# Kernel optimization log

Hardware: AMD Instinct MI355X
Metric: run time of the kernel (lower is better)

The kernel has to match this reference:

```python
import jax, jax.numpy as jnp
import numpy as np

N_NODES = 50000
N_EDGES = 800000
NFEAT = 512
NHID = 64
NHEADS = 8
NCLASS = 40
ALPHA = 0.2  # LeakyReLU slope
EPS = 1e-16  # guards isolated-node division


def setup_inputs() -> dict:
    key = jax.random.key(0)
    k = jax.random.split(key, 6)
    x = jax.random.normal(k[0], (N_NODES, NFEAT), dtype=jnp.float32)
    W_heads = jax.random.normal(k[1], (NHEADS, NFEAT, NHID), dtype=jnp.float32) * 0.05
    a_heads = jax.random.normal(k[2], (NHEADS, 2 * NHID), dtype=jnp.float32) * 0.05
    W_out = jax.random.normal(k[3], (NHEADS * NHID, NCLASS), dtype=jnp.float32) * 0.05
    a_out = jax.random.normal(k[4], (2 * NCLASS,), dtype=jnp.float32) * 0.05
    edge_index = jax.random.randint(k[5], (2, N_EDGES), 0, N_NODES, dtype=jnp.int32)
    return {"x": x, "W_heads": W_heads, "a_heads": a_heads,
            "W_out": W_out, "a_out": a_out, "edge_index": edge_index}


def _gat_layer(x, W, a, row, col, concat):
    # pyGAT sparse layer: h = xW; e_ij = exp(-LeakyReLU(a^T [h_i || h_j]));
    # out_i = sum_j e_ij h_j / sum_j e_ij   (aggregate into row, gather from col)
    D = W.shape[1]
    h = x @ W                                            # [N, D]
    score = h[row] @ a[:D] + h[col] @ a[D:]              # [E]
    e = jnp.exp(-jax.nn.leaky_relu(score, ALPHA))        # [E]
    num = jax.ops.segment_sum(e[:, None] * h[col], row, num_segments=x.shape[0])  # [N, D]
    den = jax.ops.segment_sum(e, row, num_segments=x.shape[0])                    # [N]
    out = num / (den[:, None] + EPS)
    return jax.nn.elu(out) if concat else out


def reference(x, W_heads, a_heads, W_out, a_out, edge_index):
    # dropout layers are identity in eval mode (training=False)
    row, col = edge_index[0], edge_index[1]
    heads = jax.vmap(lambda W, a: _gat_layer(x, W, a, row, col, True))(W_heads, a_heads)
    # [H, N, D] -> [N, H*D] (concat along feature dim, head-major like torch.cat)
    hcat = jnp.transpose(heads, (1, 0, 2)).reshape(x.shape[0], -1)
    return _gat_layer(hcat, W_out, a_out, row, col, False)  # [N, NCLASS]
```

## Files before the change

### kernel.cpp

```cpp
#include <hip/hip_runtime.h>
#include <hip/hip_bf16.h>

#define N_NODES 50000
#define N_EDGES 800000
#define NFEAT   512
#define NHID    64
#define NHEADS  8
#define NCLASS  40
#define HD      (NHEADS*NHID)
#define ALPHA   0.2f
#define EPS_F   1e-16f
#define NCHUNK  ((N_NODES + 255)/256)

typedef __attribute__((ext_vector_type(8))) short short8;
typedef __attribute__((ext_vector_type(4))) float floatx4;

__device__ __forceinline__ float bf2f(unsigned short u) {
    union { unsigned int i; float f; } v; v.i = ((unsigned int)u) << 16; return v.f;
}
__device__ __forceinline__ unsigned short f2bf(float f) {
    union { __hip_bfloat16 h; unsigned short u; } cv;
    cv.h = __float2bfloat16(f);
    return cv.u;
}

__device__ __forceinline__ void gload16(const unsigned short* g, short* l) {
    __builtin_amdgcn_global_load_lds(
        (const __attribute__((address_space(1))) void*)g,
        (__attribute__((address_space(3))) void*)l,
        16, 0, 0);
}

__global__ __launch_bounds__(256) void convx(const float* __restrict__ x,
                                             unsigned short* __restrict__ xb) {
    int i = blockIdx.x*256 + threadIdx.x;
    if (i >= N_NODES*64) return;
    const float* s = x + (size_t)i*8;
    float4 a = *(const float4*)s, b = *(const float4*)(s+4);
    short8 h;
    h[0] = (short)f2bf(a.x); h[1] = (short)f2bf(a.y);
    h[2] = (short)f2bf(a.z); h[3] = (short)f2bf(a.w);
    h[4] = (short)f2bf(b.x); h[5] = (short)f2bf(b.y);
    h[6] = (short)f2bf(b.z); h[7] = (short)f2bf(b.w);
    *(short8*)(xb + (size_t)i*8) = h;
}

__global__ void prep(const float* __restrict__ Wh, unsigned short* __restrict__ Wrb,
                     const float* __restrict__ Wo, unsigned short* __restrict__ Wob,
                     int* __restrict__ deg) {
    int idx = blockIdx.x*256 + threadIdx.x;
    if (idx >= 512*512) return;
    if (idx < N_NODES) deg[idx] = 0;
    {
        int n = idx >> 9, k = idx & 511;
        int hd = n >> 6, d = n & 63;
        Wrb[idx] = f2bf(Wh[(size_t)hd*NFEAT*NHID + (size_t)k*NHID + d]);
    }
    if (idx < 64*512) {
        int n = idx >> 9, k = idx & 511;
        float v = (n < NCLASS) ? Wo[(size_t)k*NCLASS + n] : 0.f;
        Wob[idx] = f2bf(v);
    }
}

__global__ __launch_bounds__(256) void mfma_gemm1(const unsigned short* __restrict__ Abf,
                                                  const unsigned short* __restrict__ Bbf,
                                                  const float* __restrict__ a_heads,
                                                  unsigned short* __restrict__ H1p,
                                                  float* __restrict__ srcdot,
                                                  float* __restrict__ dstdot, int M) {
    int id = blockIdx.x;
    int rb = (id >> 5)*8 + (id & 7);
    int cb = (id >> 3) & 3;
    int row0 = rb * 128, col0 = cb * 128;
    if (row0 >= M) return;

    __shared__ short Asl[128*32];
    __shared__ short Bsl[128*32];
    int tid  = threadIdx.x;
    int wid  = tid >> 6, lane = tid & 63;
    int lrow = lane & 15, quad = lane >> 4;
    int wm = wid & 1, wn = wid >> 1;

    int srow = wid*16 + (lane >> 2);
    int skk  = (lane & 3) * 8;
    int ar0 = row0 + srow;      ar0 = ar0 < M ? ar0 : M - 1;
    int ar1 = row0 + 64 + srow; ar1 = ar1 < M ? ar1 : M - 1;
    const unsigned short* ag0 = Abf + (size_t)ar0*512 + skk;
    const unsigned short* ag1 = Abf + (size_t)ar1*512 + skk;
    const unsigned short* bg0 = Bbf + (size_t)(col0 + srow)*512 + skk;
    const unsigned short* bg1 = Bbf + (size_t)(col0 + 64 + srow)*512 + skk;
    short* al0 = &Asl[(wid*16)*32];
    short* al1 = &Asl[(64 + wid*16)*32];
    short* bl0 = &Bsl[(wid*16)*32];
    short* bl1 = &Bsl[(64 + wid*16)*32];

    floatx4 acc[4][4];
#pragma unroll
    for (int mm = 0; mm < 4; mm++)
#pragma unroll
        for (int nn = 0; nn < 4; nn++) acc[mm][nn] = (floatx4){0.f,0.f,0.f,0.f};

    for (int k0 = 0; k0 < 512; k0 += 32) {
        gload16(ag0 + k0, al0);
        gload16(ag1 + k0, al1);
        gload16(bg0 + k0, bl0);
        gload16(bg1 + k0, bl1);
        __syncthreads();
        short8 af[4], bfr[4];
#pragma unroll
        for (int mm = 0; mm < 4; ++mm)
            af[mm] = *(const short8*)(&Asl[(wm*64 + mm*16 + lrow)*32 + quad*8]);
#pragma unroll
        for (int nn = 0; nn < 4; ++nn)
            bfr[nn] = *(const short8*)(&Bsl[(wn*64 + nn*16 + lrow)*32 + quad*8]);
#pragma unroll
        for (int mm = 0; mm < 4; ++mm)
#pragma unroll
            for (int nn = 0; nn < 4; ++nn)
                acc[mm][nn] = __builtin_amdgcn_mfma_f32_16x16x32_bf16(
                    af[mm], bfr[nn], acc[mm][nn], 0, 0, 0);
        __syncthreads();
    }

    {
        int head = (col0 >> 6) + wn;
        float a0v[4], a1v[4];
#pragma unroll
        for (int nn = 0; nn < 4; ++nn) {
            a0v[nn] = a_heads[head*128 + nn*16 + lrow];
            a1v[nn] = a_heads[head*128 + 64 + nn*16 + lrow];
        }
#pragma unroll
        for (int mm = 0; mm < 4; ++mm) {
#pragma unroll
            for (int r = 0; r < 4; ++r) {
                float s0 = 0.f, s1 = 0.f;
#pragma unroll
                for (int nn = 0; nn < 4; ++nn) {
                    float v = acc[mm][nn][r];
                    s0 = fmaf(v, a0v[nn], s0);
                    s1 = fmaf(v, a1v[nn], s1);
                }
#pragma unroll
                for (int off = 1; off < 16; off <<= 1) {
                    s0 += __shfl_xor(s0, off, 64);
                    s1 += __shfl_xor(s1, off, 64);
                }
                int grow = row0 + wm*64 + mm*16 + quad*4 + r;
                if (lrow == 0 && grow < M) {
                    srcdot[(size_t)grow*8 + head] = s0;
                    dstdot[(size_t)grow*8 + head] = s1;
                }
            }
        }
    }

#pragma unroll
    for (int mm = 0; mm < 4; ++mm) {
        int rbase = row0 + wm*64 + mm*16 + quad*4;
#pragma unroll
        for (int nn = 0; nn < 4; ++nn) {
            int c = col0 + wn*64 + nn*16 + lrow;
            int off = (c & 63)*8 + (c >> 6);
#pragma unroll
            for (int r = 0; r < 4; ++r) {
                int grow = rbase + r;
                if (grow < M)
                    H1p[(size_t)grow*512 + off] = f2bf(acc[mm][nn][r]);
            }
        }
    }
}

__global__ __launch_bounds__(512) void mfma_gemm2(const unsigned short* __restrict__ Abf,
                                                  const unsigned short* __restrict__ Bbf,
                                                  const float* __restrict__ a_out,
                                                  float* __restrict__ H2p,
                                                  float* __restrict__ src2,
                                                  float* __restrict__ dst2, int M) {
    __shared__ short Asl[128*32];
    __shared__ short Bsl[64*32];
    int tid  = threadIdx.x;
    int wid  = tid >> 6, lane = tid & 63;
    int lrow = lane & 15, quad = lane >> 4;
    int row0 = blockIdx.x * 128;
    if (row0 >= M) return;

    int srow = wid*16 + (lane >> 2);
    int skk  = (lane & 3) * 8;
    int ar = row0 + srow; ar = ar < M ? ar : M - 1;
    const unsigned short* ag = Abf + (size_t)ar*512 + skk;
    const unsigned short* bg = Bbf + (size_t)srow*512 + skk;
    short* al = &Asl[(wid*16)*32];
    short* bl = &Bsl[(wid*16)*32];

    floatx4 acc[4];
#pragma unroll
    for (int nn = 0; nn < 4; nn++) acc[nn] = (floatx4){0.f,0.f,0.f,0.f};

    for (int k0 = 0; k0 < 512; k0 += 32) {
        gload16(ag + k0, al);
        if (wid < 4) gload16(bg + k0, bl);
        __syncthreads();
        short8 af, bfr[4];
        af = *(const short8*)(&Asl[(wid*16 + lrow)*32 + quad*8]);
#pragma unroll
        for (int nn = 0; nn < 4; ++nn)
            bfr[nn] = *(const short8*)(&Bsl[(nn*16 + lrow)*32 + quad*8]);
#pragma unroll
        for (int nn = 0; nn < 4; ++nn)
            acc[nn] = __builtin_amdgcn_mfma_f32_16x16x32_bf16(
                af, bfr[nn], acc[nn], 0, 0, 0);
        __syncthreads();
    }

    {
        float a0v[4], a1v[4];
#pragma unroll
        for (int nn = 0; nn < 4; ++nn) {
            int c = nn*16 + lrow;
            a0v[nn] = c < NCLASS ? a_out[c] : 0.f;
            a1v[nn] = c < NCLASS ? a_out[NCLASS + c] : 0.f;
        }
#pragma unroll
        for (int r = 0; r < 4; ++r) {
            float s0 = 0.f, s1 = 0.f;
#pragma unroll
            for (int nn = 0; nn < 4; ++nn) {
                float v = acc[nn][r];
                s0 = fmaf(v, a0v[nn], s0);
                s1 = fmaf(v, a1v[nn], s1);
            }
#pragma unroll
            for (int off = 1; off < 16; off <<= 1) {
                s0 += __shfl_xor(s0, off, 64);
                s1 += __shfl_xor(s1, off, 64);
            }
            int grow = row0 + wid*16 + quad*4 + r;
            if (lrow == 0 && grow < M) {
                src2[grow] = s0;
                dst2[grow] = s1;
            }
        }
    }

#pragma unroll
    for (int nn = 0; nn < 4; ++nn) {
        int c = nn*16 + lrow;
#pragma unroll
        for (int r = 0; r < 4; ++r) {
            int grow = row0 + wid*16 + quad*4 + r;
            if (grow < M)
                H2p[(size_t)grow*64 + c] = acc[nn][r];
        }
    }
}

__global__ void histk(const int* __restrict__ row, int* __restrict__ deg) {
    int e = blockIdx.x*256 + threadIdx.x;
    if (e < N_EDGES) atomicAdd(&deg[row[e]], 1);
}
__global__ void scanA(const int* __restrict__ deg, int* __restrict__ row_ptr,
                      int* __restrict__ chunk_tot) {
    __shared__ int s[256];
    int t = threadIdx.x;
    int idx = blockIdx.x*256 + t;
    int v = (idx < N_NODES) ? deg[idx] : 0;
    s[t] = v;
    __syncthreads();
#pragma unroll
    for (int off = 1; off < 256; off <<= 1) {
        int x = (t >= off) ? s[t-off] : 0;
        __syncthreads();
        s[t] += x;
        __syncthreads();
    }
    if (idx < N_NODES) row_ptr[idx] = s[t] - v;
    if (t == 255) chunk_tot[blockIdx.x] = s[t];
}
__global__ void scanB(const int* __restrict__ chunk_tot, int* __restrict__ chunk_off,
                      int* __restrict__ row_ptr) {
    __shared__ int s[256];
    int t = threadIdx.x;
    int v = (t < NCHUNK) ? chunk_tot[t] : 0;
    s[t] = v;
    __syncthreads();
#pragma unroll
    for (int off = 1; off < 256; off <<= 1) {
        int x = (t >= off) ? s[t-off] : 0;
        __syncthreads();
        s[t] += x;
        __syncthreads();
    }
    if (t < NCHUNK) chunk_off[t] = s[t] - v;
    if (t == 255) row_ptr[N_NODES] = s[t];
}
__global__ void scanC(const int* __restrict__ chunk_off, int* __restrict__ row_ptr,
                      int* __restrict__ cursor) {
    int idx = blockIdx.x*256 + threadIdx.x;
    if (idx < N_NODES) {
        int rp = row_ptr[idx] + chunk_off[idx >> 8];
        row_ptr[idx] = rp;
        cursor[idx] = rp;
    }
}

__global__ void fillk_w1(const int* __restrict__ row, const int* __restrict__ col,
                         const float* __restrict__ srcdot, const float* __restrict__ dstdot,
                         int* __restrict__ cursor, int* __restrict__ csr_col,
                         float* __restrict__ Wcsr) {
    int e = blockIdx.x*256 + threadIdx.x;
    if (e >= N_EDGES) return;
    int r = row[e], c = col[e];
    int pos = atomicAdd(&cursor[r], 1);
    csr_col[pos] = c;
    float4 sa = *(const float4*)(srcdot + (size_t)r*8);
    float4 sb = *(const float4*)(srcdot + (size_t)r*8 + 4);
    float4 da = *(const float4*)(dstdot + (size_t)c*8);
    float4 db = *(const float4*)(dstdot + (size_t)c*8 + 4);
    float s[8] = {sa.x+da.x, sa.y+da.y, sa.z+da.z, sa.w+da.w,
                  sb.x+db.x, sb.y+db.y, sb.z+db.z, sb.w+db.w};
    float o[8];
#pragma unroll
    for (int j = 0; j < 8; j++) {
        float lr = s[j] > 0.f ? s[j] : ALPHA*s[j];
        o[j] = __expf(-lr);
    }
    *(float4*)(Wcsr + (size_t)pos*8)     = make_float4(o[0], o[1], o[2], o[3]);
    *(float4*)(Wcsr + (size_t)pos*8 + 4) = make_float4(o[4], o[5], o[6], o[7]);
}

__global__ __launch_bounds__(256) void agg1(const unsigned short* __restrict__ H1p,
                                            const float* __restrict__ Wcsr,
                                            const int* __restrict__ row_ptr,
                                            const int* __restrict__ csr_col,
                                            unsigned short* __restrict__ hcatb) {
    int wave = (blockIdx.x*256 + threadIdx.x) >> 6;
    int lane = threadIdx.x & 63;
    if (wave >= N_NODES) return;
    int start = row_ptr[wave], end = row_ptr[wave+1];
    float acc[8], den[8];
#pragma unroll
    for (int j = 0; j < 8; j++) { acc[j] = 0.f; den[j] = 0.f; }

    int k = start;
    for (; k + 4 <= end; k += 4) {
        int c0 = csr_col[k],   c1 = csr_col[k+1];
        int c2 = csr_col[k+2], c3 = csr_col[k+3];
        short8 hv0 = *(const short8*)(H1p + (size_t)c0*512 + lane*8);
        short8 hv1 = *(const short8*)(H1p + (size_t)c1*512 + lane*8);
        short8 hv2 = *(const short8*)(H1p + (size_t)c2*512 + lane*8);
        short8 hv3 = *(const short8*)(H1p + (size_t)c3*512 + lane*8);
        float4 wv[8];
#pragma unroll
        for (int q = 0; q < 8; q++)
            wv[q] = *(const float4*)(Wcsr + (size_t)k*8 + q*4);
        const float* w0 = (const float*)&wv[0];
        const float* w1 = (const float*)&wv[2];
        const float* w2 = (const float*)&wv[4];
        const float* w3 = (const float*)&wv[6];
#pragma unroll
        for (int j = 0; j < 8; j++) {
            den[j] += (w0[j] + w1[j]) + (w2[j] + w3[j]);
            acc[j] = fmaf(w0[j], bf2f((unsigned short)hv0[j]), acc[j]);
            acc[j] = fmaf(w1[j], bf2f((unsigned short)hv1[j]), acc[j]);
            acc[j] = fmaf(w2[j], bf2f((unsigned short)hv2[j]), acc[j]);
            acc[j] = fmaf(w3[j], bf2f((unsigned short)hv3[j]), acc[j]);
        }
    }
    for (; k < end; ++k) {
        int c = csr_col[k];
        float4 wa = *(const float4*)(Wcsr + (size_t)k*8);
        float4 wb = *(const float4*)(Wcsr + (size_t)k*8 + 4);
        short8 hv = *(const short8*)(H1p + (size_t)c*512 + lane*8);
        float w[8] = {wa.x, wa.y, wa.z, wa.w, wb.x, wb.y, wb.z, wb.w};
#pragma unroll
        for (int j = 0; j < 8; j++) {
            den[j] += w[j];
            acc[j] = fmaf(w[j], bf2f((unsigned short)hv[j]), acc[j]);
        }
    }
#pragma unroll
    for (int j = 0; j < 8; j++) {
        float o = acc[j] / (den[j] + EPS_F);
        o = o > 0.f ? o : (__expf(o) - 1.f);
        hcatb[(size_t)wave*HD + j*64 + lane] = f2bf(o);
    }
}

__global__ __launch_bounds__(256) void agg2(const float* __restrict__ H2p,
                                            const float* __restrict__ src2,
                                            const float* __restrict__ dst2,
                                            const int* __restrict__ row_ptr,
                                            const int* __restrict__ csr_col,
                                            float* __restrict__ out) {
    int wave = (blockIdx.x*256 + threadIdx.x) >> 6;
    int lane = threadIdx.x & 63;
    if (wave >= N_NODES) return;
    int start = row_ptr[wave], end = row_ptr[wave+1];
    int deg = end - start;
    float s2i = src2[wave];
    int l = lane < NCLASS ? lane : 0;
    float acc = 0.f, den = 0.f;

    int colreg = 0;
    if (deg > 0) colreg = csr_col[start + (lane < deg ? lane : deg - 1)];

#define AG2_G1(T, H, IDX) do { \
    int cg_ = __builtin_amdgcn_readlane(colreg, (IDX)); \
    T = dst2[cg_]; \
    H = H2p[(size_t)cg_*64 + l]; \
} while(0)
#define AG2_C1(T, H) do { \
    float t_ = s2i + (T); \
    t_ = t_ > 0.f ? t_ : ALPHA*t_; \
    float w_ = __expf(-t_); \
    den += w_; acc = fmaf(w_, (H), acc); \
} while(0)
#define AG2_G8(T0,T1,T2,T3,T4,T5,T6,T7,H0,H1,H2,H3,H4,H5,H6,H7,BASE) do { \
    AG2_G1(T0,H0,(BASE));   AG2_G1(T1,H1,(BASE)+1); \
    AG2_G1(T2,H2,(BASE)+2); AG2_G1(T3,H3,(BASE)+3); \
    AG2_G1(T4,H4,(BASE)+4); AG2_G1(T5,H5,(BASE)+5); \
    AG2_G1(T6,H6,(BASE)+6); AG2_G1(T7,H7,(BASE)+7); \
} while(0)
#define AG2_C8(T0,T1,T2,T3,T4,T5,T6,T7,H0,H1,H2,H3,H4,H5,H6,H7) do { \
    AG2_C1(T0,H0); AG2_C1(T1,H1); AG2_C1(T2,H2); AG2_C1(T3,H3); \
    AG2_C1(T4,H4); AG2_C1(T5,H5); AG2_C1(T6,H6); AG2_C1(T7,H7); \
} while(0)

    int lim = deg < 64 ? deg : 64;
    int nb = lim >> 3;
    int k = start;
    float ta0,ta1,ta2,ta3,ta4,ta5,ta6,ta7, ga0,ga1,ga2,ga3,ga4,ga5,ga6,ga7;
    float tb0,tb1,tb2,tb3,tb4,tb5,tb6,tb7, gb0,gb1,gb2,gb3,gb4,gb5,gb6,gb7;
    if (nb > 0) {
        AG2_G8(ta0,ta1,ta2,ta3,ta4,ta5,ta6,ta7, ga0,ga1,ga2,ga3,ga4,ga5,ga6,ga7, 0);
        int b = 1;
        for (; b + 1 < nb; b += 2) {
            AG2_G8(tb0,tb1,tb2,tb3,tb4,tb5,tb6,tb7, gb0,gb1,gb2,gb3,gb4,gb5,gb6,gb7, b*8);
            AG2_C8(ta0,ta1,ta2,ta3,ta4,ta5,ta6,ta7, ga0,ga1,ga2,ga3,ga4,ga5,ga6,ga7);
            AG2_G8(ta0,ta1,ta2,ta3,ta4,ta5,ta6,ta7, ga0,ga1,ga2,ga3,ga4,ga5,ga6,ga7, (b+1)*8);
            AG2_C8(tb0,tb1,tb2,tb3,tb4,tb5,tb6,tb7, gb0,gb1,gb2,gb3,gb4,gb5,gb6,gb7);
        }
        if (b < nb) {
            AG2_G8(tb0,tb1,tb2,tb3,tb4,tb5,tb6,tb7, gb0,gb1,gb2,gb3,gb4,gb5,gb6,gb7, b*8);
            AG2_C8(ta0,ta1,ta2,ta3,ta4,ta5,ta6,ta7, ga0,ga1,ga2,ga3,ga4,ga5,ga6,ga7);
            AG2_C8(tb0,tb1,tb2,tb3,tb4,tb5,tb6,tb7, gb0,gb1,gb2,gb3,gb4,gb5,gb6,gb7);
        } else {
            AG2_C8(ta0,ta1,ta2,ta3,ta4,ta5,ta6,ta7, ga0,ga1,ga2,ga3,ga4,ga5,ga6,ga7);
        }
        k = start + nb*8;
    }
    for (; k < end; ++k) {
        int c_ = (k - start < 64) ? __builtin_amdgcn_readlane(colreg, k - start)
                                  : csr_col[k];
        float t = dst2[c_];
        float h = H2p[(size_t)c_*64 + l];
        AG2_C1(t, h);
    }
#undef AG2_G1
#undef AG2_C1
#undef AG2_G8
#undef AG2_C8

    if (lane < NCLASS)
        out[(size_t)wave*NCLASS + lane] = acc / (den + EPS_F);
}

extern "C" void kernel_launch(void* const* d_in, const int* in_sizes, int n_in,
                              void* d_out, int out_size, void* d_ws, size_t ws_size,
                              hipStream_t stream) {
    const float* x       = (const float*)d_in[0];
    const float* W_heads = (const float*)d_in[1];
    const float* a_heads = (const float*)d_in[2];
    const float* W_out   = (const float*)d_in[3];
    const float* a_out   = (const float*)d_in[4];
    const int*   ei      = (const int*)d_in[5];
    const int*   row     = ei;
    const int*   col     = ei + N_EDGES;
    float* out = (float*)d_out;

    char* ws = (char*)d_ws;
    size_t off = 0;
    auto alloc = [&](size_t bytes) {
        char* p = ws + off;
        off = (off + bytes + 255) & ~(size_t)255;
        return p;
    };
    unsigned short* Wrb   = (unsigned short*)alloc((size_t)512*512*2);
    unsigned short* Wob   = (unsigned short*)alloc((size_t)64*512*2);
    unsigned short* H1p   = (unsigned short*)alloc((size_t)N_NODES*HD*2);
    unsigned short* xb    = (unsigned short*)alloc((size_t)N_NODES*NFEAT*2);
    unsigned short* hcatb = xb;
    float* srcdot  = (float*)alloc((size_t)N_NODES*NHEADS*4);
    float* dstdot  = (float*)alloc((size_t)N_NODES*NHEADS*4);
    float* Wcsr    = (float*)alloc((size_t)N_EDGES*NHEADS*4);
    int*   deg     = (int*)alloc((size_t)N_NODES*4);
    int*   row_ptr = (int*)alloc((size_t)(N_NODES+1)*4);
    int*   cursor  = (int*)alloc((size_t)N_NODES*4);
    int*   ctot    = (int*)alloc(256*4);
    int*   coff    = (int*)alloc(256*4);
    int*   csr_col = (int*)alloc((size_t)N_EDGES*4);
    float* H2p     = (float*)alloc((size_t)N_NODES*64*4);
    float* src2    = (float*)alloc((size_t)N_NODES*4);
    float* dst2    = (float*)alloc((size_t)N_NODES*4);
    (void)ws_size;

    const int EB = (N_EDGES + 255)/256;
    const int WB = (N_NODES*64 + 255)/256;

    prep<<<(512*512 + 255)/256, 256, 0, stream>>>(W_heads, Wrb, W_out, Wob, deg);
    convx<<<(N_NODES*64 + 255)/256, 256, 0, stream>>>(x, xb);
    {
        int rtiles = (N_NODES + 127)/128;
        int nblk = ((rtiles + 7)/8) * 32;
        mfma_gemm1<<<nblk, 256, 0, stream>>>(xb, Wrb, a_heads, H1p,
                                             srcdot, dstdot, N_NODES);
    }

    histk<<<EB, 256, 0, stream>>>(row, deg);
    scanA<<<NCHUNK, 256, 0, stream>>>(deg, row_ptr, ctot);
    scanB<<<1, 256, 0, stream>>>(ctot, coff, row_ptr);
    scanC<<<NCHUNK, 256, 0, stream>>>(coff, row_ptr, cursor);
    fillk_w1<<<EB, 256, 0, stream>>>(row, col, srcdot, dstdot, cursor,
                                     csr_col, Wcsr);

    agg1<<<WB, 256, 0, stream>>>(H1p, Wcsr, row_ptr, csr_col, hcatb);

    mfma_gemm2<<<(N_NODES + 127)/128, 512, 0, stream>>>(hcatb, Wob, a_out,
                                                        H2p, src2, dst2, N_NODES);
    agg2<<<WB, 256, 0, stream>>>(H2p, src2, dst2, row_ptr, csr_col, out);
}
```

Measured before the change: 509.0 us.

## Store H1 head-major, give each agg1 lane one head, fuse convx into prep

The GEMM1 epilogue now writes H1 in natural head-major column order instead of an interleaved per-lane layout. In agg1 each lane handles 8 contiguous features of a single head, so it loads only one attention weight per edge instead of eight. It also keeps one denominator and one reciprocal instead of eight divisions, and writes its output as a single 16-byte vector store. The x-to-bf16 conversion is merged into the prep kernel to save a launch, and the gemm2 B-tile LDS pointer is clamped with wid&3 for the waves that skip the B load.

```diff
diff --git a/kernel.cpp b/kernel.cpp
--- a/kernel.cpp
+++ b/kernel.cpp
@@ -31,27 +31,26 @@
         16, 0, 0);
 }
 
-__global__ __launch_bounds__(256) void convx(const float* __restrict__ x,
-                                             unsigned short* __restrict__ xb) {
-    int i = blockIdx.x*256 + threadIdx.x;
-    if (i >= N_NODES*64) return;
-    const float* s = x + (size_t)i*8;
-    float4 a = *(const float4*)s, b = *(const float4*)(s+4);
-    short8 h;
-    h[0] = (short)f2bf(a.x); h[1] = (short)f2bf(a.y);
-    h[2] = (short)f2bf(a.z); h[3] = (short)f2bf(a.w);
-    h[4] = (short)f2bf(b.x); h[5] = (short)f2bf(b.y);
-    h[6] = (short)f2bf(b.z); h[7] = (short)f2bf(b.w);
-    *(short8*)(xb + (size_t)i*8) = h;
-}
-
-__global__ void prep(const float* __restrict__ Wh, unsigned short* __restrict__ Wrb,
-                     const float* __restrict__ Wo, unsigned short* __restrict__ Wob,
-                     int* __restrict__ deg) {
+__global__ __launch_bounds__(256) void prep(const float* __restrict__ x,
+                                            unsigned short* __restrict__ xb,
+                                            const float* __restrict__ Wh,
+                                            unsigned short* __restrict__ Wrb,
+                                            const float* __restrict__ Wo,
+                                            unsigned short* __restrict__ Wob,
+                                            int* __restrict__ deg) {
     int idx = blockIdx.x*256 + threadIdx.x;
-    if (idx >= 512*512) return;
+    if (idx < N_NODES*64) {
+        const float* s = x + (size_t)idx*8;
+        float4 a = *(const float4*)s, b = *(const float4*)(s+4);
+        short8 h;
+        h[0] = (short)f2bf(a.x); h[1] = (short)f2bf(a.y);
+        h[2] = (short)f2bf(a.z); h[3] = (short)f2bf(a.w);
+        h[4] = (short)f2bf(b.x); h[5] = (short)f2bf(b.y);
+        h[6] = (short)f2bf(b.z); h[7] = (short)f2bf(b.w);
+        *(short8*)(xb + (size_t)idx*8) = h;
+    }
     if (idx < N_NODES) deg[idx] = 0;
-    {
+    if (idx < 512*512) {
         int n = idx >> 9, k = idx & 511;
         int hd = n >> 6, d = n & 63;
         Wrb[idx] = f2bf(Wh[(size_t)hd*NFEAT*NHID + (size_t)k*NHID + d]);
@@ -66,7 +65,7 @@
 __global__ __launch_bounds__(256) void mfma_gemm1(const unsigned short* __restrict__ Abf,
                                                   const unsigned short* __restrict__ Bbf,
                                                   const float* __restrict__ a_heads,
-                                                  unsigned short* __restrict__ H1p,
+                                                  unsigned short* __restrict__ H1,
                                                   float* __restrict__ srcdot,
                                                   float* __restrict__ dstdot, int M) {
     int id = blockIdx.x;
@@ -160,14 +159,14 @@
     for (int mm = 0; mm < 4; ++mm) {
         int rbase = row0 + wm*64 + mm*16 + quad*4;
 #pragma unroll
-        for (int nn = 0; nn < 4; ++nn) {
-            int c = col0 + wn*64 + nn*16 + lrow;
-            int off = (c & 63)*8 + (c >> 6);
-#pragma unroll
-            for (int r = 0; r < 4; ++r) {
-                int grow = rbase + r;
-                if (grow < M)
-                    H1p[(size_t)grow*512 + off] = f2bf(acc[mm][nn][r]);
+        for (int r = 0; r < 4; ++r) {
+            int grow = rbase + r;
+            if (grow < M) {
+#pragma unroll
+                for (int nn = 0; nn < 4; ++nn) {
+                    int c = col0 + wn*64 + nn*16 + lrow;
+                    H1[(size_t)grow*512 + c] = f2bf(acc[mm][nn][r]);
+                }
             }
         }
     }
@@ -193,7 +192,7 @@
     const unsigned short* ag = Abf + (size_t)ar*512 + skk;
     const unsigned short* bg = Bbf + (size_t)srow*512 + skk;
     short* al = &Asl[(wid*16)*32];
-    short* bl = &Bsl[(wid*16)*32];
+    short* bl = &Bsl[((wid & 3)*16)*32];
 
     floatx4 acc[4];
 #pragma unroll
@@ -331,7 +330,7 @@
     *(float4*)(Wcsr + (size_t)pos*8 + 4) = make_float4(o[4], o[5], o[6], o[7]);
 }
 
-__global__ __launch_bounds__(256) void agg1(const unsigned short* __restrict__ H1p,
+__global__ __launch_bounds__(256) void agg1(const unsigned short* __restrict__ H1,
                                             const float* __restrict__ Wcsr,
                                             const int* __restrict__ row_ptr,
                                             const int* __restrict__ csr_col,
@@ -340,53 +339,51 @@
     int lane = threadIdx.x & 63;
     if (wave >= N_NODES) return;
     int start = row_ptr[wave], end = row_ptr[wave+1];
-    float acc[8], den[8];
-#pragma unroll
-    for (int j = 0; j < 8; j++) { acc[j] = 0.f; den[j] = 0.f; }
+    int hd = lane >> 3;
+    float acc[8];
+    float den = 0.f;
+#pragma unroll
+    for (int j = 0; j < 8; j++) acc[j] = 0.f;
 
     int k = start;
     for (; k + 4 <= end; k += 4) {
         int c0 = csr_col[k],   c1 = csr_col[k+1];
         int c2 = csr_col[k+2], c3 = csr_col[k+3];
-        short8 hv0 = *(const short8*)(H1p + (size_t)c0*512 + lane*8);
-        short8 hv1 = *(const short8*)(H1p + (size_t)c1*512 + lane*8);
-        short8 hv2 = *(const short8*)(H1p + (size_t)c2*512 + lane*8);
-        short8 hv3 = *(const short8*)(H1p + (size_t)c3*512 + lane*8);
-        float4 wv[8];
-#pragma unroll
-        for (int q = 0; q < 8; q++)
-            wv[q] = *(const float4*)(Wcsr + (size_t)k*8 + q*4);
-        const float* w0 = (const float*)&wv[0];
-        const float* w1 = (const float*)&wv[2];
-        const float* w2 = (const float*)&wv[4];
-        const float* w3 = (const float*)&wv[6];
+        short8 hv0 = *(const short8*)(H1 + (size_t)c0*512 + lane*8);
+        short8 hv1 = *(const short8*)(H1 + (size_t)c1*512 + lane*8);
+        short8 hv2 = *(const short8*)(H1 + (size_t)c2*512 + lane*8);
+        short8 hv3 = *(const short8*)(H1 + (size_t)c3*512 + lane*8);
+        float w0 = Wcsr[(size_t)(k+0)*8 + hd];
+        float w1 = Wcsr[(size_t)(k+1)*8 + hd];
+        float w2 = Wcsr[(size_t)(k+2)*8 + hd];
+        float w3 = Wcsr[(size_t)(k+3)*8 + hd];
+        den += (w0 + w1) + (w2 + w3);
 #pragma unroll
         for (int j = 0; j < 8; j++) {
-            den[j] += (w0[j] + w1[j]) + (w2[j] + w3[j]);
-            acc[j] = fmaf(w0[j], bf2f((unsigned short)hv0[j]), acc[j]);
-            acc[j] = fmaf(w1[j], bf2f((unsigned short)hv1[j]), acc[j]);
-            acc[j] = fmaf(w2[j], bf2f((unsigned short)hv2[j]), acc[j]);
-            acc[j] = fmaf(w3[j], bf2f((unsigned short)hv3[j]), acc[j]);
+            acc[j] = fmaf(w0, bf2f((unsigned short)hv0[j]), acc[j]);
+            acc[j] = fmaf(w1, bf2f((unsigned short)hv1[j]), acc[j]);
+            acc[j] = fmaf(w2, bf2f((unsigned short)hv2[j]), acc[j]);
+            acc[j] = fmaf(w3, bf2f((unsigned short)hv3[j]), acc[j]);
         }
     }
     for (; k < end; ++k) {
         int c = csr_col[k];
-        float4 wa = *(const float4*)(Wcsr + (size_t)k*8);
-        float4 wb = *(const float4*)(Wcsr + (size_t)k*8 + 4);
-        short8 hv = *(const short8*)(H1p + (size_t)c*512 + lane*8);
-        float w[8] = {wa.x, wa.y, wa.z, wa.w, wb.x, wb.y, wb.z, wb.w};
-#pragma unroll
-        for (int j = 0; j < 8; j++) {
-            den[j] += w[j];
-            acc[j] = fmaf(w[j], bf2f((unsigned short)hv[j]), acc[j]);
-        }
-    }
+        short8 hv = *(const short8*)(H1 + (size_t)c*512 + lane*8);
+        float w = Wcsr[(size_t)k*8 + hd];
+        den += w;
+#pragma unroll
+        for (int j = 0; j < 8; j++)
+            acc[j] = fmaf(w, bf2f((unsigned short)hv[j]), acc[j]);
+    }
+    float rden = 1.f / (den + EPS_F);
+    short8 o8;
 #pragma unroll
     for (int j = 0; j < 8; j++) {
-        float o = acc[j] / (den[j] + EPS_F);
+        float o = acc[j] * rden;
         o = o > 0.f ? o : (__expf(o) - 1.f);
-        hcatb[(size_t)wave*HD + j*64 + lane] = f2bf(o);
-    }
+        o8[j] = (short)f2bf(o);
+    }
+    *(short8*)(hcatb + (size_t)wave*HD + lane*8) = o8;
 }
 
 __global__ __launch_bounds__(256) void agg2(const float* __restrict__ H2p,
@@ -490,7 +487,7 @@
     };
     unsigned short* Wrb   = (unsigned short*)alloc((size_t)512*512*2);
     unsigned short* Wob   = (unsigned short*)alloc((size_t)64*512*2);
-    unsigned short* H1p   = (unsigned short*)alloc((size_t)N_NODES*HD*2);
+    unsigned short* H1    = (unsigned short*)alloc((size_t)N_NODES*HD*2);
     unsigned short* xb    = (unsigned short*)alloc((size_t)N_NODES*NFEAT*2);
     unsigned short* hcatb = xb;
     float* srcdot  = (float*)alloc((size_t)N_NODES*NHEADS*4);
@@ -510,12 +507,12 @@
     const int EB = (N_EDGES + 255)/256;
     const int WB = (N_NODES*64 + 255)/256;
 
-    prep<<<(512*512 + 255)/256, 256, 0, stream>>>(W_heads, Wrb, W_out, Wob, deg);
-    convx<<<(N_NODES*64 + 255)/256, 256, 0, stream>>>(x, xb);
+    prep<<<(N_NODES*64 + 255)/256, 256, 0, stream>>>(x, xb, W_heads, Wrb,
+                                                     W_out, Wob, deg);
     {
         int rtiles = (N_NODES + 127)/128;
         int nblk = ((rtiles + 7)/8) * 32;
-        mfma_gemm1<<<nblk, 256, 0, stream>>>(xb, Wrb, a_heads, H1p,
+        mfma_gemm1<<<nblk, 256, 0, stream>>>(xb, Wrb, a_heads, H1,
                                              srcdot, dstdot, N_NODES);
     }
 
@@ -526,7 +523,7 @@
     fillk_w1<<<EB, 256, 0, stream>>>(row, col, srcdot, dstdot, cursor,
                                      csr_col, Wcsr);
 
-    agg1<<<WB, 256, 0, stream>>>(H1p, Wcsr, row_ptr, csr_col, hcatb);
+    agg1<<<WB, 256, 0, stream>>>(H1, Wcsr, row_ptr, csr_col, hcatb);
 
     mfma_gemm2<<<(N_NODES + 127)/128, 512, 0, stream>>>(hcatb, Wob, a_out,
                                                         H2p, src2, dst2, N_NODES);
```

Result: faster. 486.6 us (-4.4%).
